# Performance work log

Hardware: AMD Instinct MI355X
Metric: run time of the kernel (lower is better)

Reference implementation:

```python
import jax, jax.numpy as jnp
import numpy as np


def setup_inputs() -> dict:
    key = jax.random.key(0)
    ks = jax.random.split(key, 10)
    B, C, T, H, W = 8, 128, 8, 32, 32
    Cq = C // 8
    return {
        "x": jax.random.normal(ks[0], (B, C, T, H, W), dtype=jnp.float32),
        "Wq": jax.random.normal(ks[1], (Cq, C), dtype=jnp.float32) * (1.0 / np.sqrt(C)),
        "bq": jax.random.normal(ks[2], (Cq,), dtype=jnp.float32) * 0.02,
        "Wk": jax.random.normal(ks[3], (Cq, C), dtype=jnp.float32) * (1.0 / np.sqrt(C)),
        "bk": jax.random.normal(ks[4], (Cq,), dtype=jnp.float32) * 0.02,
        "Wv": jax.random.normal(ks[5], (C, C), dtype=jnp.float32) * (1.0 / np.sqrt(C)),
        "bv": jax.random.normal(ks[6], (C,), dtype=jnp.float32) * 0.02,
        "gamma_pam": jax.random.normal(ks[7], (1,), dtype=jnp.float32),
        "gamma_cam": jax.random.normal(ks[8], (1,), dtype=jnp.float32),
        "gamma_tim": jax.random.normal(ks[9], (1,), dtype=jnp.float32),
    }


def reference(x, Wq, bq, Wk, bk, Wv, bv, gamma_pam, gamma_cam, gamma_tim):
    B, C, T, H, W = x.shape
    HW = H * W

    # ---- PAM: position attention over HW, feature dim = (C//8)*T ----
    # 1x1x1 Conv3d == per-position channel matmul
    q = jnp.einsum('bcthw,oc->bothw', x, Wq) + bq[None, :, None, None, None]
    k = jnp.einsum('bcthw,oc->bothw', x, Wk) + bk[None, :, None, None, None]
    v = jnp.einsum('bcthw,oc->bothw', x, Wv) + bv[None, :, None, None, None]
    qf = q.reshape(B, -1, HW)   # [B, (C//8)*T, HW]
    kf = k.reshape(B, -1, HW)
    vf = v.reshape(B, -1, HW)   # [B, C*T, HW]
    energy = jnp.einsum('bcn,bcm->bnm', qf, kf)          # [B, HW, HW]
    attn = jax.nn.softmax(energy, axis=-1)
    # out = bmm(v, attn^T)
    pam = jnp.einsum('bcm,bnm->bcn', vf, attn).reshape(B, C, T, H, W)
    pam = gamma_pam * pam + x

    # ---- CAM: channel attention (C x C) with negated-energy softmax ----
    xc = x.reshape(B, C, -1)                              # [B, C, T*HW]
    e = jnp.einsum('bcn,bdn->bcd', xc, xc)                # [B, C, C]
    e = jnp.max(e, axis=-1, keepdims=True) - e
    a = jax.nn.softmax(e, axis=-1)
    cam = jnp.einsum('bcd,bdn->bcn', a, xc).reshape(B, C, T, H, W)
    cam = gamma_cam * cam + x

    # ---- TIM: temporal attention (T x T) with negated-energy softmax ----
    xt = jnp.transpose(x, (0, 2, 1, 3, 4)).reshape(B, T, -1)  # [B, T, C*HW]
    e = jnp.einsum('btn,bsn->bts', xt, xt)                # [B, T, T]
    e = jnp.max(e, axis=-1, keepdims=True) - e
    a = jax.nn.softmax(e, axis=-1)
    tim = jnp.einsum('bts,bsn->btn', a, xt).reshape(B, T, C, H, W)
    tim = jnp.transpose(tim, (0, 2, 1, 3, 4))
    tim = gamma_tim * tim + x

    return pam + cam + tim
```

## Files before the change

### kernel.cpp

```cpp
#include <hip/hip_runtime.h>
#include <cstdint>

typedef unsigned short u16;
typedef __attribute__((ext_vector_type(8))) short bf16x8;
typedef __attribute__((ext_vector_type(4))) float f32x4;

constexpr int B_  = 8;
constexpr int C_  = 128;
constexpr int T_  = 8;
constexpr int HW_ = 1024;
constexpr int P_  = T_ * HW_;
constexpr int F_  = 128;
constexpr int CT_ = C_ * T_;

static __device__ __forceinline__ u16 f2bf(float f) {
    union { float f; unsigned u; } v; v.f = f;
    unsigned r = v.u + 0x7fffu + ((v.u >> 16) & 1u);
    return (u16)(r >> 16);
}
static __device__ __forceinline__ float bf2f(u16 h) {
    union { unsigned u; float f; } v; v.u = ((unsigned)h) << 16;
    return v.f;
}

#define GLOAD16(src, dst)                                                     \
    __builtin_amdgcn_global_load_lds(                                         \
        (const __attribute__((address_space(1))) void*)(src),                 \
        (__attribute__((address_space(3))) void*)(dst), 16, 0, 0)

__global__ __launch_bounds__(256)
void k_wcast(const float* __restrict__ Wq, const float* __restrict__ bq,
             const float* __restrict__ Wk, const float* __restrict__ bk,
             const float* __restrict__ Wv, const float* __restrict__ bv,
             u16* __restrict__ Wall, float* __restrict__ ball)
{
    int tid = blockIdx.x * 256 + threadIdx.x;
    if (tid < 20480) {
        int oc = tid >> 7, c = tid & 127;
        float w;
        if (oc < 16)      w = Wq[oc * 128 + c];
        else if (oc < 32) w = Wk[(oc - 16) * 128 + c];
        else              w = Wv[(oc - 32) * 128 + c];
        Wall[tid] = f2bf(w);
    }
    if (tid < 160) {
        float bb;
        if (tid < 16)      bb = bq[tid];
        else if (tid < 32) bb = bk[tid - 16];
        else               bb = bv[tid - 32];
        ball[tid] = bb;
    }
}

__global__ __launch_bounds__(256)
void k_prep(const float* __restrict__ x, u16* __restrict__ xT)
{
    __shared__ char sy[32768];
    const int b  = blockIdx.y;
    const int p0 = blockIdx.x * 128;
    const int tid = threadIdx.x;

    #pragma unroll
    for (int r = 0; r < 16; r++) {
        int lin = r * 256 + tid;
        int c = lin >> 5, j4 = (lin & 31) << 2;
        float4 xv = *(const float4*)&x[((size_t)(b * C_ + c)) * P_ + p0 + j4];
        float a4[4] = {xv.x, xv.y, xv.z, xv.w};
        #pragma unroll
        for (int u = 0; u < 4; u++) {
            int pi = j4 + u;
            int byte = pi * 256 + ((c * 2) ^ (((pi >> 2) & 15) << 4));
            *(u16*)(sy + byte) = f2bf(a4[u]);
        }
    }
    __syncthreads();
    #pragma unroll
    for (int r = 0; r < 8; r++) {
        int lin = r * 256 + tid;
        int pi = lin >> 4, ci8 = (lin & 15) << 3;
        bf16x8 v = *(const bf16x8*)(sy + pi * 256 +
                                    ((ci8 * 2) ^ (((pi >> 2) & 15) << 4)));
        *(bf16x8*)&xT[((size_t)(b * P_ + p0 + pi)) * C_ + ci8] = v;
    }
}

__global__ __launch_bounds__(256)
void k_qkv(const u16* __restrict__ xT, const u16* __restrict__ Wall,
           const float* __restrict__ ball,
           u16* __restrict__ qt, u16* __restrict__ kt, u16* __restrict__ v16)
{
    __shared__ char Ws[40960];
    const int b  = blockIdx.y;
    const int p0 = blockIdx.x * 128;
    const int tid = threadIdx.x, lane = tid & 63, w = tid >> 6;

    #pragma unroll
    for (int i = 0; i < 10; i++) {
        int ch  = w * 10 + i;
        int row = ch * 4 + (lane >> 4);
        int col = ((lane & 15) ^ (row & 7)) * 8;
        GLOAD16(Wall + row * 128 + col, Ws + ch * 1024);
    }

    const u16* Bb = xT + ((size_t)(b * P_ + p0 + w * 32)) * F_;
    bf16x8 bg[4][2];
    #pragma unroll
    for (int ks = 0; ks < 4; ks++)
        #pragma unroll
        for (int ni = 0; ni < 2; ni++)
            bg[ks][ni] = *(const bf16x8*)(Bb +
                (size_t)(ni * 16 + (lane & 15)) * F_ + ks * 32 + (lane >> 4) * 8);
    __syncthreads();

    f32x4 acc[10][2];
    #pragma unroll
    for (int mi = 0; mi < 10; mi++) {
        acc[mi][0] = (f32x4){0.f, 0.f, 0.f, 0.f};
        acc[mi][1] = (f32x4){0.f, 0.f, 0.f, 0.f};
    }

    #pragma unroll
    for (int mi = 0; mi < 10; mi++) {
        #pragma unroll
        for (int ks = 0; ks < 4; ks++) {
            int row  = mi * 16 + (lane & 15);
            int slot = (ks * 4 + (lane >> 4)) ^ (row & 7);
            bf16x8 af = *(const bf16x8*)(Ws + row * 256 + slot * 16);
            acc[mi][0] = __builtin_amdgcn_mfma_f32_16x16x32_bf16(
                af, bg[ks][0], acc[mi][0], 0, 0, 0);
            acc[mi][1] = __builtin_amdgcn_mfma_f32_16x16x32_bf16(
                af, bg[ks][1], acc[mi][1], 0, 0, 0);
        }
    }

    const int t      = p0 >> 10;
    const int hwbase = (p0 & 1023) + w * 32;
    #pragma unroll
    for (int mi = 0; mi < 10; mi++)
        #pragma unroll
        for (int ni = 0; ni < 2; ni++)
            #pragma unroll
            for (int r = 0; r < 4; r++) {
                int oc = mi * 16 + (lane >> 4) * 4 + r;
                int hw = hwbase + ni * 16 + (lane & 15);
                u16 bv16 = f2bf(acc[mi][ni][r] + ball[oc]);
                if (mi == 0)
                    qt[((size_t)b * HW_ + hw) * F_ + oc * 8 + t] = bv16;
                else if (mi == 1)
                    kt[((size_t)b * HW_ + hw) * F_ + (oc - 16) * 8 + t] = bv16;
                else
                    v16[((size_t)(b * C_ + oc - 32)) * P_ + t * HW_ + hw] = bv16;
            }
}

__global__ __launch_bounds__(256)
void k_energy(const u16* __restrict__ qt, const u16* __restrict__ kt,
              float* __restrict__ E)
{
    __shared__ char As[32768];
    __shared__ char Bs[32768];
    const int b  = blockIdx.z;
    const int n0 = blockIdx.y * 128, m0 = blockIdx.x * 128;
    const int tid = threadIdx.x, lane = tid & 63, w = tid >> 6;
    const u16* qb = qt + (size_t)b * HW_ * F_;
    const u16* kb = kt + (size_t)b * HW_ * F_;

    #pragma unroll
    for (int i = 0; i < 8; i++) {
        int c    = w * 8 + i;
        int row  = c * 4 + (lane >> 4);
        int col  = ((lane & 15) ^ (row & 7)) * 8;
        GLOAD16(qb + (size_t)(n0 + row) * F_ + col, As + c * 1024);
        GLOAD16(kb + (size_t)(m0 + row) * F_ + col, Bs + c * 1024);
    }
    __syncthreads();

    const int wr = w >> 1, wc = w & 1;
    f32x4 acc[4][4];
    #pragma unroll
    for (int mi = 0; mi < 4; mi++)
        #pragma unroll
        for (int ni = 0; ni < 4; ni++) acc[mi][ni] = (f32x4){0.f, 0.f, 0.f, 0.f};

    #pragma unroll
    for (int ks = 0; ks < 4; ks++) {
        bf16x8 af[4], bg[4];
        #pragma unroll
        for (int mi = 0; mi < 4; mi++) {
            int row  = wr * 64 + mi * 16 + (lane & 15);
            int slot = (ks * 4 + (lane >> 4)) ^ (row & 7);
            af[mi] = *(const bf16x8*)(As + row * 256 + slot * 16);
            int rb  = wc * 64 + mi * 16 + (lane & 15);
            int sb  = (ks * 4 + (lane >> 4)) ^ (rb & 7);
            bg[mi] = *(const bf16x8*)(Bs + rb * 256 + sb * 16);
        }
        #pragma unroll
        for (int mi = 0; mi < 4; mi++)
            #pragma unroll
            for (int ni = 0; ni < 4; ni++)
                acc[mi][ni] = __builtin_amdgcn_mfma_f32_16x16x32_bf16(
                    af[mi], bg[ni], acc[mi][ni], 0, 0, 0);
    }

    float* Eb = E + (size_t)b * HW_ * HW_;
    #pragma unroll
    for (int mi = 0; mi < 4; mi++)
        #pragma unroll
        for (int ni = 0; ni < 4; ni++)
            #pragma unroll
            for (int r = 0; r < 4; r++)
                Eb[(size_t)(n0 + wr * 64 + mi * 16 + (lane >> 4) * 4 + r) * HW_
                   + m0 + wc * 64 + ni * 16 + (lane & 15)] = acc[mi][ni][r];
}

__global__ __launch_bounds__(256)
void k_softmax(const float* __restrict__ E, u16* __restrict__ A16)
{
    const float* e = E + (size_t)blockIdx.x * HW_;
    const int tid = threadIdx.x;
    float4 v = ((const float4*)e)[tid];
    float m = fmaxf(fmaxf(v.x, v.y), fmaxf(v.z, v.w));
    #pragma unroll
    for (int off = 32; off; off >>= 1) m = fmaxf(m, __shfl_xor(m, off));
    __shared__ float s1[4], s2[4];
    if ((tid & 63) == 0) s1[tid >> 6] = m;
    __syncthreads();
    m = fmaxf(fmaxf(s1[0], s1[1]), fmaxf(s1[2], s1[3]));
    v.x = __expf(v.x - m); v.y = __expf(v.y - m);
    v.z = __expf(v.z - m); v.w = __expf(v.w - m);
    float s = v.x + v.y + v.z + v.w;
    #pragma unroll
    for (int off = 32; off; off >>= 1) s += __shfl_xor(s, off);
    if ((tid & 63) == 0) s2[tid >> 6] = s;
    __syncthreads();
    s = s2[0] + s2[1] + s2[2] + s2[3];
    float inv = 1.0f / s;
    ushort4 pk;
    pk.x = f2bf(v.x * inv); pk.y = f2bf(v.y * inv);
    pk.z = f2bf(v.z * inv); pk.w = f2bf(v.w * inv);
    ((ushort4*)(A16 + (size_t)blockIdx.x * HW_))[tid] = pk;
}

__global__ __launch_bounds__(256)
void k_pv(const u16* __restrict__ v16, const u16* __restrict__ A16,
          const float* __restrict__ gamma_pam, float* __restrict__ out)
{
    __shared__ char As[16384];
    __shared__ char Bs[16384];
    const int b   = blockIdx.z;
    const int ct0 = blockIdx.y * 128, n0 = blockIdx.x * 128;
    const int tid = threadIdx.x, lane = tid & 63, w = tid >> 6;
    const u16* vb = v16 + (size_t)b * CT_ * HW_;
    const u16* ab = A16 + (size_t)b * HW_ * HW_;

    const int wr = w >> 1, wc = w & 1;
    f32x4 acc[4][4];
    #pragma unroll
    for (int mi = 0; mi < 4; mi++)
        #pragma unroll
        for (int ni = 0; ni < 4; ni++) acc[mi][ni] = (f32x4){0.f, 0.f, 0.f, 0.f};

    for (int mc = 0; mc < 1024; mc += 64) {
        #pragma unroll
        for (int i = 0; i < 4; i++) {
            int c   = w * 4 + i;
            int row = c * 8 + (lane >> 3);
            int col = ((lane & 7) ^ (row & 7)) * 8;
            GLOAD16(vb + (size_t)(ct0 + row) * HW_ + mc + col, As + c * 1024);
            GLOAD16(ab + (size_t)(n0  + row) * HW_ + mc + col, Bs + c * 1024);
        }
        __syncthreads();
        #pragma unroll
        for (int ks = 0; ks < 2; ks++) {
            bf16x8 af[4], bg[4];
            #pragma unroll
            for (int mi = 0; mi < 4; mi++) {
                int row  = wr * 64 + mi * 16 + (lane & 15);
                int slot = (ks * 4 + (lane >> 4)) ^ (row & 7);
                af[mi] = *(const bf16x8*)(As + row * 128 + slot * 16);
                int rb  = wc * 64 + mi * 16 + (lane & 15);
                int sb  = (ks * 4 + (lane >> 4)) ^ (rb & 7);
                bg[mi] = *(const bf16x8*)(Bs + rb * 128 + sb * 16);
            }
            #pragma unroll
            for (int mi = 0; mi < 4; mi++)
                #pragma unroll
                for (int ni = 0; ni < 4; ni++)
                    acc[mi][ni] = __builtin_amdgcn_mfma_f32_16x16x32_bf16(
                        af[mi], bg[ni], acc[mi][ni], 0, 0, 0);
        }
        __syncthreads();
    }

    const float gp = gamma_pam[0];
    float* ob = out + (size_t)b * CT_ * HW_;
    #pragma unroll
    for (int mi = 0; mi < 4; mi++)
        #pragma unroll
        for (int ni = 0; ni < 4; ni++)
            #pragma unroll
            for (int r = 0; r < 4; r++)
                ob[(size_t)(ct0 + wr * 64 + mi * 16 + (lane >> 4) * 4 + r) * HW_
                   + n0 + wc * 64 + ni * 16 + (lane & 15)] = gp * acc[mi][ni][r];
}

__global__ __launch_bounds__(256)
void k_split(const float* __restrict__ x, u16* __restrict__ xhi,
             u16* __restrict__ xlo)
{
    for (int i = blockIdx.x * 256 + threadIdx.x; i < 2097152; i += 2048 * 256) {
        float4 v = ((const float4*)x)[i];
        ushort4 h, l;
        h.x = f2bf(v.x); h.y = f2bf(v.y); h.z = f2bf(v.z); h.w = f2bf(v.w);
        l.x = f2bf(v.x - bf2f(h.x)); l.y = f2bf(v.y - bf2f(h.y));
        l.z = f2bf(v.z - bf2f(h.z)); l.w = f2bf(v.w - bf2f(h.w));
        ((ushort4*)xhi)[i] = h;
        ((ushort4*)xlo)[i] = l;
    }
}

__global__ __launch_bounds__(256)
void k_cam_gram(const u16* __restrict__ xhi, const u16* __restrict__ xlo,
                float* __restrict__ part)
{
    __shared__ char Sh[32768];
    __shared__ char Sl[32768];
    const int b = blockIdx.y, ch = blockIdx.x;
    const int tid = threadIdx.x, lane = tid & 63, w = tid >> 6;
    const u16* hb = xhi + (size_t)b * C_ * P_;
    const u16* lb = xlo + (size_t)b * C_ * P_;

    f32x4 acc[8][2];
    #pragma unroll
    for (int mi = 0; mi < 8; mi++) {
        acc[mi][0] = (f32x4){0.f, 0.f, 0.f, 0.f};
        acc[mi][1] = (f32x4){0.f, 0.f, 0.f, 0.f};
    }

    for (int kc = 0; kc < 2; kc++) {
        int n0 = ch * 256 + kc * 128;
        #pragma unroll
        for (int i = 0; i < 8; i++) {
            int c4  = w * 8 + i;
            int row = c4 * 4 + (lane >> 4);
            int col = ((lane & 15) ^ (row & 7)) * 8;
            GLOAD16(hb + (size_t)row * P_ + n0 + col, Sh + c4 * 1024);
            GLOAD16(lb + (size_t)row * P_ + n0 + col, Sl + c4 * 1024);
        }
        __syncthreads();
        #pragma unroll
        for (int ks = 0; ks < 4; ks++) {
            bf16x8 bh[2], bl[2];
            #pragma unroll
            for (int ni = 0; ni < 2; ni++) {
                int rb = w * 32 + ni * 16 + (lane & 15);
                int sb = (ks * 4 + (lane >> 4)) ^ (rb & 7);
                bh[ni] = *(const bf16x8*)(Sh + rb * 256 + sb * 16);
                bl[ni] = *(const bf16x8*)(Sl + rb * 256 + sb * 16);
            }
            #pragma unroll
            for (int mi = 0; mi < 8; mi++) {
                int ra = mi * 16 + (lane & 15);
                int sa = (ks * 4 + (lane >> 4)) ^ (ra & 7);
                bf16x8 ah = *(const bf16x8*)(Sh + ra * 256 + sa * 16);
                bf16x8 al = *(const bf16x8*)(Sl + ra * 256 + sa * 16);
                #pragma unroll
                for (int ni = 0; ni < 2; ni++) {
                    acc[mi][ni] = __builtin_amdgcn_mfma_f32_16x16x32_bf16(
                        ah, bh[ni], acc[mi][ni], 0, 0, 0);
                    acc[mi][ni] = __builtin_amdgcn_mfma_f32_16x16x32_bf16(
                        ah, bl[ni], acc[mi][ni], 0, 0, 0);
                    acc[mi][ni] = __builtin_amdgcn_mfma_f32_16x16x32_bf16(
                        al, bh[ni], acc[mi][ni], 0, 0, 0);
                }
            }
        }
        __syncthreads();
    }

    float* pb = part + ((size_t)(b * 32 + ch)) * 16384;
    #pragma unroll
    for (int mi = 0; mi < 8; mi++)
        #pragma unroll
        for (int ni = 0; ni < 2; ni++)
            #pragma unroll
            for (int r = 0; r < 4; r++) {
                int c = mi * 16 + (lane >> 4) * 4 + r;
                int d = w * 32 + ni * 16 + (lane & 15);
                pb[c * 128 + d] = acc[mi][ni][r];
            }
}

__global__ __launch_bounds__(128)
void k_cam_reduce(const float* __restrict__ part,
                  const float* __restrict__ gamma_cam, u16* __restrict__ acam16)
{
    const int b = blockIdx.y, c = blockIdx.x;
    const int d = threadIdx.x;
    float s = 0.f;
    for (int ch = 0; ch < 32; ch++)
        s += part[(((size_t)(b * 32 + ch)) * C_ + c) * C_ + d];
    float mn = s;
    #pragma unroll
    for (int off = 32; off; off >>= 1) mn = fminf(mn, __shfl_xor(mn, off));
    __shared__ float m1[2], m2[2];
    if ((d & 63) == 0) m1[d >> 6] = mn;
    __syncthreads();
    mn = fminf(m1[0], m1[1]);
    float p = __expf(mn - s);
    float sum = p;
    #pragma unroll
    for (int off = 32; off; off >>= 1) sum += __shfl_xor(sum, off);
    if ((d & 63) == 0) m2[d >> 6] = sum;
    __syncthreads();
    sum = m2[0] + m2[1];
    acam16[((size_t)(b * C_ + c)) * C_ + d] = f2bf(gamma_cam[0] * p / sum);
}

__global__ __launch_bounds__(256)
void k_tim_gram(const float* __restrict__ x, float* __restrict__ e_t)
{
    const int b = blockIdx.y, c = blockIdx.x;
    const int tid = threadIdx.x;
    const float* xb = x + ((size_t)(b * C_ + c)) * P_;
    float acc[8][8] = {};
    for (int r = 0; r < 4; r++) {
        int hw = r * 256 + tid;
        float xv[8];
        #pragma unroll
        for (int t = 0; t < 8; t++) xv[t] = xb[t * HW_ + hw];
        #pragma unroll
        for (int t = 0; t < 8; t++)
            #pragma unroll
            for (int s2 = 0; s2 < 8; s2++)
                acc[t][s2] += xv[t] * xv[s2];
    }
    __shared__ float sm[4][64];
    const int lane = tid & 63, wid = tid >> 6;
    #pragma unroll
    for (int u = 0; u < 64; u++) {
        float vv = acc[u >> 3][u & 7];
        #pragma unroll
        for (int off = 32; off; off >>= 1) vv += __shfl_xor(vv, off);
        if (lane == 0) sm[wid][u] = vv;
    }
    __syncthreads();
    if (tid < 64) {
        float vv = sm[0][tid] + sm[1][tid] + sm[2][tid] + sm[3][tid];
        atomicAdd(&e_t[b * 64 + tid], vv);
    }
}

__global__ __launch_bounds__(512)
void k_tim_softmax(const float* __restrict__ e_t, float* __restrict__ a_t)
{
    const int tid = threadIdx.x;
    float v = e_t[tid];
    float mn = v;
    #pragma unroll
    for (int off = 4; off; off >>= 1) mn = fminf(mn, __shfl_xor(mn, off, 8));
    float p = __expf(mn - v);
    float s = p;
    #pragma unroll
    for (int off = 4; off; off >>= 1) s += __shfl_xor(s, off, 8);
    a_t[tid] = p / s;
}

__global__ __launch_bounds__(256)
void k_xprime(const float* __restrict__ x, const float* __restrict__ atim,
              const float* __restrict__ gamma_tim, u16* __restrict__ Xp)
{
    const int b = blockIdx.y, c = blockIdx.x;
    const size_t base = ((size_t)(b * C_ + c)) * P_;
    const int tid = threadIdx.x;
    const float gt = gamma_tim[0];

    float4 xv[8];
    #pragma unroll
    for (int t = 0; t < 8; t++)
        xv[t] = *(const float4*)&x[base + t * HW_ + tid * 4];

    #pragma unroll
    for (int t = 0; t < 8; t++) {
        float4 o = make_float4(3.f * xv[t].x, 3.f * xv[t].y,
                               3.f * xv[t].z, 3.f * xv[t].w);
        #pragma unroll
        for (int s = 0; s < 8; s++) {
            float w = gt * atim[b * 64 + t * 8 + s];
            o.x += w * xv[s].x; o.y += w * xv[s].y;
            o.z += w * xv[s].z; o.w += w * xv[s].w;
        }
        ushort4 pk;
        pk.x = f2bf(o.x); pk.y = f2bf(o.y); pk.z = f2bf(o.z); pk.w = f2bf(o.w);
        *(ushort4*)&Xp[base + t * HW_ + tid * 4] = pk;
    }
}

__global__ __launch_bounds__(256)
void k_cam_av(const u16* __restrict__ acam16, const u16* __restrict__ xT,
              const u16* __restrict__ Xp, float* __restrict__ out)
{
    const int b  = blockIdx.y;
    const int p0 = blockIdx.x * 128;
    const int tid = threadIdx.x, lane = tid & 63, w = tid >> 6;

    const u16* Ab = acam16 + (size_t)b * C_ * C_;
    const u16* Bb = xT + ((size_t)(b * P_ + p0 + w * 32)) * C_;

    f32x4 acc[8][2];
    #pragma unroll
    for (int mi = 0; mi < 8; mi++) {
        acc[mi][0] = (f32x4){0.f, 0.f, 0.f, 0.f};
        acc[mi][1] = (f32x4){0.f, 0.f, 0.f, 0.f};
    }

    bf16x8 bg[4][2];
    #pragma unroll
    for (int ks = 0; ks < 4; ks++)
        #pragma unroll
        for (int ni = 0; ni < 2; ni++)
            bg[ks][ni] = *(const bf16x8*)(Bb +
                (size_t)(ni * 16 + (lane & 15)) * C_ + ks * 32 + (lane >> 4) * 8);

    #pragma unroll
    for (int mi = 0; mi < 8; mi++) {
        #pragma unroll
        for (int ks = 0; ks < 4; ks++) {
            bf16x8 af = *(const bf16x8*)(Ab +
                (size_t)(mi * 16 + (lane & 15)) * C_ + ks * 32 + (lane >> 4) * 8);
            acc[mi][0] = __builtin_amdgcn_mfma_f32_16x16x32_bf16(
                af, bg[ks][0], acc[mi][0], 0, 0, 0);
            acc[mi][1] = __builtin_amdgcn_mfma_f32_16x16x32_bf16(
                af, bg[ks][1], acc[mi][1], 0, 0, 0);
        }
    }

    float* ob = out + (size_t)b * C_ * P_;
    const u16* xp = Xp + (size_t)b * C_ * P_;
    #pragma unroll
    for (int mi = 0; mi < 8; mi++)
        #pragma unroll
        for (int ni = 0; ni < 2; ni++)
            #pragma unroll
            for (int r = 0; r < 4; r++) {
                int c = mi * 16 + (lane >> 4) * 4 + r;
                int p = p0 + w * 32 + ni * 16 + (lane & 15);
                size_t i = (size_t)c * P_ + p;
                ob[i] += acc[mi][ni][r] + bf2f(xp[i]);
            }
}

extern "C" void kernel_launch(void* const* d_in, const int* in_sizes, int n_in,
                              void* d_out, int out_size, void* d_ws, size_t ws_size,
                              hipStream_t stream)
{
    (void)in_sizes; (void)n_in; (void)out_size; (void)ws_size;
    const float* x  = (const float*)d_in[0];
    const float* Wq = (const float*)d_in[1];
    const float* bq = (const float*)d_in[2];
    const float* Wk = (const float*)d_in[3];
    const float* bk = (const float*)d_in[4];
    const float* Wv = (const float*)d_in[5];
    const float* bv = (const float*)d_in[6];
    const float* gp = (const float*)d_in[7];
    const float* gc = (const float*)d_in[8];
    const float* gt = (const float*)d_in[9];
    float* out = (float*)d_out;
    char*  ws  = (char*)d_ws;

    const size_t MiB = 1u << 20;
    u16*   xT     = (u16*)(ws + 0);
    u16*   qtb    = (u16*)(ws + 16 * MiB);
    u16*   ktb    = (u16*)(ws + 18 * MiB);
    u16*   v16    = (u16*)(ws + 20 * MiB);
    u16*   Xp16   = (u16*)(ws + 20 * MiB);
    float* Ebuf   = (float*)(ws + 36 * MiB);
    u16*   xhi    = (u16*)(ws + 36 * MiB);
    u16*   xlo    = (u16*)(ws + 52 * MiB);
    u16*   A16    = (u16*)(ws + 68 * MiB);
    float* part   = (float*)(ws + 68 * MiB);
    u16*   acam16 = (u16*)(ws + 84 * MiB);
    u16*   Wall   = (u16*)(ws + 84 * MiB + 65536);
    float* ball   = (float*)(ws + 84 * MiB + 131072);
    float* etim   = (float*)(ws + 84 * MiB + 139264);
    float* atim   = (float*)(ws + 84 * MiB + 143360);

    hipMemsetAsync(etim, 0, 512 * sizeof(float), stream);

    k_wcast      <<<dim3(80),      256, 0, stream>>>(Wq, bq, Wk, bk, Wv, bv,
                                                     Wall, ball);
    k_prep       <<<dim3(64, 8),   256, 0, stream>>>(x, xT);
    k_qkv        <<<dim3(64, 8),   256, 0, stream>>>(xT, Wall, ball,
                                                     qtb, ktb, v16);
    k_energy     <<<dim3(8, 8, 8), 256, 0, stream>>>(qtb, ktb, Ebuf);
    k_softmax    <<<dim3(8192),    256, 0, stream>>>(Ebuf, A16);
    k_split      <<<dim3(2048),    256, 0, stream>>>(x, xhi, xlo);
    k_tim_gram   <<<dim3(128, 8),  256, 0, stream>>>(x, etim);
    k_tim_softmax<<<dim3(1),       512, 0, stream>>>(etim, atim);
    k_pv         <<<dim3(8, 8, 8), 256, 0, stream>>>(v16, A16, gp, out);
    k_xprime     <<<dim3(128, 8),  256, 0, stream>>>(x, atim, gt, Xp16);
    k_cam_gram   <<<dim3(32, 8),   256, 0, stream>>>(xhi, xlo, part);
    k_cam_reduce <<<dim3(128, 8),  128, 0, stream>>>(part, gc, acam16);
    k_cam_av     <<<dim3(64, 8),   256, 0, stream>>>(acam16, xT, Xp16, out);
}
```

Baseline: 263.4 us.

## Fuse prep kernels, double-buffer PV GEMM, and store PAM as bf16

Folds the weight cast and the hi/lo bf16 split of x into the prep kernel, and moves the temporal softmax into k_xprime. This removes three launches and one full extra pass over x. The PV GEMM now double-buffers its LDS tiles so global loads for the next step overlap the MFMA work on the current one. PAM output is written as bf16 to a scratch buffer and added in the final CAM kernel, which replaces the fp32 read-modify-write of out with a single store. The cost is reduced PAM precision, twice the LDS in k_pv, and a strided gather of PAM values in the epilogue.

New measurement: 266.1 us. No clear change (+1.0%).

```diff
diff --git a/kernel.cpp b/kernel.cpp
--- a/kernel.cpp
+++ b/kernel.cpp
@@ -29,48 +29,58 @@
         (__attribute__((address_space(3))) void*)(dst), 16, 0, 0)
 
 __global__ __launch_bounds__(256)
-void k_wcast(const float* __restrict__ Wq, const float* __restrict__ bq,
-             const float* __restrict__ Wk, const float* __restrict__ bk,
-             const float* __restrict__ Wv, const float* __restrict__ bv,
-             u16* __restrict__ Wall, float* __restrict__ ball)
-{
-    int tid = blockIdx.x * 256 + threadIdx.x;
-    if (tid < 20480) {
-        int oc = tid >> 7, c = tid & 127;
-        float w;
-        if (oc < 16)      w = Wq[oc * 128 + c];
-        else if (oc < 32) w = Wk[(oc - 16) * 128 + c];
-        else              w = Wv[(oc - 32) * 128 + c];
-        Wall[tid] = f2bf(w);
-    }
-    if (tid < 160) {
-        float bb;
-        if (tid < 16)      bb = bq[tid];
-        else if (tid < 32) bb = bk[tid - 16];
-        else               bb = bv[tid - 32];
-        ball[tid] = bb;
-    }
-}
-
-__global__ __launch_bounds__(256)
-void k_prep(const float* __restrict__ x, u16* __restrict__ xT)
-{
+void k_prep(const float* __restrict__ x, u16* __restrict__ xT,
+            u16* __restrict__ xhi, u16* __restrict__ xlo,
+            const float* __restrict__ Wq, const float* __restrict__ bq,
+            const float* __restrict__ Wk, const float* __restrict__ bk,
+            const float* __restrict__ Wv, const float* __restrict__ bv,
+            u16* __restrict__ Wall, float* __restrict__ ball)
+{
+    const int tid = threadIdx.x;
+    if (blockIdx.x == 64) {
+        if (blockIdx.y != 0) return;
+        for (int i = tid; i < 20480; i += 256) {
+            int oc = i >> 7, c = i & 127;
+            float w;
+            if (oc < 16)      w = Wq[oc * 128 + c];
+            else if (oc < 32) w = Wk[(oc - 16) * 128 + c];
+            else              w = Wv[(oc - 32) * 128 + c];
+            Wall[i] = f2bf(w);
+        }
+        if (tid < 160) {
+            float bb;
+            if (tid < 16)      bb = bq[tid];
+            else if (tid < 32) bb = bk[tid - 16];
+            else               bb = bv[tid - 32];
+            ball[tid] = bb;
+        }
+        return;
+    }
+
     __shared__ char sy[32768];
     const int b  = blockIdx.y;
     const int p0 = blockIdx.x * 128;
-    const int tid = threadIdx.x;
 
     #pragma unroll
     for (int r = 0; r < 16; r++) {
         int lin = r * 256 + tid;
         int c = lin >> 5, j4 = (lin & 31) << 2;
-        float4 xv = *(const float4*)&x[((size_t)(b * C_ + c)) * P_ + p0 + j4];
+        size_t gi = ((size_t)(b * C_ + c)) * P_ + p0 + j4;
+        float4 xv = *(const float4*)&x[gi];
         float a4[4] = {xv.x, xv.y, xv.z, xv.w};
+        ushort4 h, l;
+        h.x = f2bf(a4[0]); h.y = f2bf(a4[1]);
+        h.z = f2bf(a4[2]); h.w = f2bf(a4[3]);
+        l.x = f2bf(a4[0] - bf2f(h.x)); l.y = f2bf(a4[1] - bf2f(h.y));
+        l.z = f2bf(a4[2] - bf2f(h.z)); l.w = f2bf(a4[3] - bf2f(h.w));
+        *(ushort4*)&xhi[gi] = h;
+        *(ushort4*)&xlo[gi] = l;
         #pragma unroll
         for (int u = 0; u < 4; u++) {
             int pi = j4 + u;
             int byte = pi * 256 + ((c * 2) ^ (((pi >> 2) & 15) << 4));
-            *(u16*)(sy + byte) = f2bf(a4[u]);
+            *(u16*)(sy + byte) = (u == 0) ? h.x : (u == 1) ? h.y
+                               : (u == 2) ? h.z : h.w;
         }
     }
     __syncthreads();
@@ -243,16 +253,19 @@
 
 __global__ __launch_bounds__(256)
 void k_pv(const u16* __restrict__ v16, const u16* __restrict__ A16,
-          const float* __restrict__ gamma_pam, float* __restrict__ out)
-{
-    __shared__ char As[16384];
-    __shared__ char Bs[16384];
+          const float* __restrict__ gamma_pam, u16* __restrict__ pam16)
+{
+    __shared__ char As[2][16384];
+    __shared__ char Bs[2][16384];
     const int b   = blockIdx.z;
     const int ct0 = blockIdx.y * 128, n0 = blockIdx.x * 128;
     const int tid = threadIdx.x, lane = tid & 63, w = tid >> 6;
     const u16* vb = v16 + (size_t)b * CT_ * HW_;
     const u16* ab = A16 + (size_t)b * HW_ * HW_;
 
+    const int s_row = (lane >> 3);
+    const int s_col = ((lane & 7) ^ ((lane >> 3) & 7)) * 8;
+
     const int wr = w >> 1, wc = w & 1;
     f32x4 acc[4][4];
     #pragma unroll
@@ -260,16 +273,31 @@
         #pragma unroll
         for (int ni = 0; ni < 4; ni++) acc[mi][ni] = (f32x4){0.f, 0.f, 0.f, 0.f};
 
-    for (int mc = 0; mc < 1024; mc += 64) {
-        #pragma unroll
-        for (int i = 0; i < 4; i++) {
-            int c   = w * 4 + i;
-            int row = c * 8 + (lane >> 3);
-            int col = ((lane & 7) ^ (row & 7)) * 8;
-            GLOAD16(vb + (size_t)(ct0 + row) * HW_ + mc + col, As + c * 1024);
-            GLOAD16(ab + (size_t)(n0  + row) * HW_ + mc + col, Bs + c * 1024);
-        }
-        __syncthreads();
+    #pragma unroll
+    for (int i = 0; i < 4; i++) {
+        int c = w * 4 + i;
+        int row = c * 8 + s_row;
+        GLOAD16(vb + (size_t)(ct0 + row) * HW_ + s_col, As[0] + c * 1024);
+        GLOAD16(ab + (size_t)(n0  + row) * HW_ + s_col, Bs[0] + c * 1024);
+    }
+    __syncthreads();
+
+    int cur = 0;
+    for (int it = 0; it < 16; ++it) {
+        if (it < 15) {
+            int mc = (it + 1) * 64;
+            #pragma unroll
+            for (int i = 0; i < 4; i++) {
+                int c = w * 4 + i;
+                int row = c * 8 + s_row;
+                GLOAD16(vb + (size_t)(ct0 + row) * HW_ + mc + s_col,
+                        As[cur ^ 1] + c * 1024);
+                GLOAD16(ab + (size_t)(n0  + row) * HW_ + mc + s_col,
+                        Bs[cur ^ 1] + c * 1024);
+            }
+        }
+        const char* Ac = As[cur];
+        const char* Bc = Bs[cur];
         #pragma unroll
         for (int ks = 0; ks < 2; ks++) {
             bf16x8 af[4], bg[4];
@@ -277,10 +305,10 @@
             for (int mi = 0; mi < 4; mi++) {
                 int row  = wr * 64 + mi * 16 + (lane & 15);
                 int slot = (ks * 4 + (lane >> 4)) ^ (row & 7);
-                af[mi] = *(const bf16x8*)(As + row * 128 + slot * 16);
+                af[mi] = *(const bf16x8*)(Ac + row * 128 + slot * 16);
                 int rb  = wc * 64 + mi * 16 + (lane & 15);
                 int sb  = (ks * 4 + (lane >> 4)) ^ (rb & 7);
-                bg[mi] = *(const bf16x8*)(Bs + rb * 128 + sb * 16);
+                bg[mi] = *(const bf16x8*)(Bc + rb * 128 + sb * 16);
             }
             #pragma unroll
             for (int mi = 0; mi < 4; mi++)
@@ -290,10 +318,11 @@
                         af[mi], bg[ni], acc[mi][ni], 0, 0, 0);
         }
         __syncthreads();
+        cur ^= 1;
     }
 
     const float gp = gamma_pam[0];
-    float* ob = out + (size_t)b * CT_ * HW_;
+    u16* ob = pam16 + (size_t)b * CT_ * HW_;
     #pragma unroll
     for (int mi = 0; mi < 4; mi++)
         #pragma unroll
@@ -301,22 +330,8 @@
             #pragma unroll
             for (int r = 0; r < 4; r++)
                 ob[(size_t)(ct0 + wr * 64 + mi * 16 + (lane >> 4) * 4 + r) * HW_
-                   + n0 + wc * 64 + ni * 16 + (lane & 15)] = gp * acc[mi][ni][r];
-}
-
-__global__ __launch_bounds__(256)
-void k_split(const float* __restrict__ x, u16* __restrict__ xhi,
-             u16* __restrict__ xlo)
-{
-    for (int i = blockIdx.x * 256 + threadIdx.x; i < 2097152; i += 2048 * 256) {
-        float4 v = ((const float4*)x)[i];
-        ushort4 h, l;
-        h.x = f2bf(v.x); h.y = f2bf(v.y); h.z = f2bf(v.z); h.w = f2bf(v.w);
-        l.x = f2bf(v.x - bf2f(h.x)); l.y = f2bf(v.y - bf2f(h.y));
-        l.z = f2bf(v.z - bf2f(h.z)); l.w = f2bf(v.w - bf2f(h.w));
-        ((ushort4*)xhi)[i] = h;
-        ((ushort4*)xlo)[i] = l;
-    }
+                   + n0 + wc * 64 + ni * 16 + (lane & 15)] =
+                    f2bf(gp * acc[mi][ni][r]);
 }
 
 __global__ __launch_bounds__(256)
@@ -451,23 +466,8 @@
     }
 }
 
-__global__ __launch_bounds__(512)
-void k_tim_softmax(const float* __restrict__ e_t, float* __restrict__ a_t)
-{
-    const int tid = threadIdx.x;
-    float v = e_t[tid];
-    float mn = v;
-    #pragma unroll
-    for (int off = 4; off; off >>= 1) mn = fminf(mn, __shfl_xor(mn, off, 8));
-    float p = __expf(mn - v);
-    float s = p;
-    #pragma unroll
-    for (int off = 4; off; off >>= 1) s += __shfl_xor(s, off, 8);
-    a_t[tid] = p / s;
-}
-
-__global__ __launch_bounds__(256)
-void k_xprime(const float* __restrict__ x, const float* __restrict__ atim,
+__global__ __launch_bounds__(256)
+void k_xprime(const float* __restrict__ x, const float* __restrict__ e_t,
               const float* __restrict__ gamma_tim, u16* __restrict__ Xp)
 {
     const int b = blockIdx.y, c = blockIdx.x;
@@ -482,13 +482,24 @@
 
     #pragma unroll
     for (int t = 0; t < 8; t++) {
+        float e[8];
+        #pragma unroll
+        for (int s = 0; s < 8; s++) e[s] = e_t[b * 64 + t * 8 + s];
+        float mn = e[0];
+        #pragma unroll
+        for (int s = 1; s < 8; s++) mn = fminf(mn, e[s]);
+        float p[8], sum = 0.f;
+        #pragma unroll
+        for (int s = 0; s < 8; s++) { p[s] = __expf(mn - e[s]); sum += p[s]; }
+        float inv = gt / sum;
+
         float4 o = make_float4(3.f * xv[t].x, 3.f * xv[t].y,
                                3.f * xv[t].z, 3.f * xv[t].w);
         #pragma unroll
         for (int s = 0; s < 8; s++) {
-            float w = gt * atim[b * 64 + t * 8 + s];
-            o.x += w * xv[s].x; o.y += w * xv[s].y;
-            o.z += w * xv[s].z; o.w += w * xv[s].w;
+            float wgt = p[s] * inv;
+            o.x += wgt * xv[s].x; o.y += wgt * xv[s].y;
+            o.z += wgt * xv[s].z; o.w += wgt * xv[s].w;
         }
         ushort4 pk;
         pk.x = f2bf(o.x); pk.y = f2bf(o.y); pk.z = f2bf(o.z); pk.w = f2bf(o.w);
@@ -498,7 +509,8 @@
 
 __global__ __launch_bounds__(256)
 void k_cam_av(const u16* __restrict__ acam16, const u16* __restrict__ xT,
-              const u16* __restrict__ Xp, float* __restrict__ out)
+              const u16* __restrict__ Xp, const u16* __restrict__ pam16,
+              float* __restrict__ out)
 {
     const int b  = blockIdx.y;
     const int p0 = blockIdx.x * 128;
@@ -535,8 +547,10 @@
         }
     }
 
+    const int tt = p0 >> 10;
     float* ob = out + (size_t)b * C_ * P_;
     const u16* xp = Xp + (size_t)b * C_ * P_;
+    const u16* pb = pam16 + (size_t)b * CT_ * HW_;
     #pragma unroll
     for (int mi = 0; mi < 8; mi++)
         #pragma unroll
@@ -545,8 +559,10 @@
             for (int r = 0; r < 4; r++) {
                 int c = mi * 16 + (lane >> 4) * 4 + r;
                 int p = p0 + w * 32 + ni * 16 + (lane & 15);
+                int hw = p & 1023;
                 size_t i = (size_t)c * P_ + p;
-                ob[i] += acc[mi][ni][r] + bf2f(xp[i]);
+                float pam = bf2f(pb[((size_t)(c * 8 + tt)) * HW_ + hw]);
+                ob[i] = pam + acc[mi][ni][r] + bf2f(xp[i]);
             }
 }
 
@@ -570,36 +586,35 @@
 
     const size_t MiB = 1u << 20;
     u16*   xT     = (u16*)(ws + 0);
-    u16*   qtb    = (u16*)(ws + 16 * MiB);
-    u16*   ktb    = (u16*)(ws + 18 * MiB);
-    u16*   v16    = (u16*)(ws + 20 * MiB);
-    u16*   Xp16   = (u16*)(ws + 20 * MiB);
-    float* Ebuf   = (float*)(ws + 36 * MiB);
-    u16*   xhi    = (u16*)(ws + 36 * MiB);
-    u16*   xlo    = (u16*)(ws + 52 * MiB);
-    u16*   A16    = (u16*)(ws + 68 * MiB);
-    float* part   = (float*)(ws + 68 * MiB);
-    u16*   acam16 = (u16*)(ws + 84 * MiB);
-    u16*   Wall   = (u16*)(ws + 84 * MiB + 65536);
-    float* ball   = (float*)(ws + 84 * MiB + 131072);
-    float* etim   = (float*)(ws + 84 * MiB + 139264);
-    float* atim   = (float*)(ws + 84 * MiB + 143360);
+    u16*   v16    = (u16*)(ws + 16 * MiB);
+    u16*   xhi    = (u16*)(ws + 32 * MiB);
+    u16*   xlo    = (u16*)(ws + 48 * MiB);
+    float* Ebuf   = (float*)(ws + 64 * MiB);
+    float* part   = (float*)(ws + 64 * MiB);
+    u16*   pam16  = (u16*)(ws + 80 * MiB);
+    u16*   A16    = (u16*)(ws + 96 * MiB);
+    u16*   Xp16   = (u16*)(ws + 96 * MiB);
+    u16*   qtb    = (u16*)(ws + 112 * MiB);
+    u16*   ktb    = (u16*)(ws + 114 * MiB);
+    u16*   acam16 = (u16*)(ws + 116 * MiB);
+    u16*   Wall   = (u16*)(ws + 116 * MiB + 65536);
+    float* ball   = (float*)(ws + 116 * MiB + 131072);
+    float* etim   = (float*)(ws + 116 * MiB + 139264);
 
     hipMemsetAsync(etim, 0, 512 * sizeof(float), stream);
 
-    k_wcast      <<<dim3(80),      256, 0, stream>>>(Wq, bq, Wk, bk, Wv, bv,
-                                                     Wall, ball);
-    k_prep       <<<dim3(64, 8),   256, 0, stream>>>(x, xT);
-    k_qkv        <<<dim3(64, 8),   256, 0, stream>>>(xT, Wall, ball,
-                                                     qtb, ktb, v16);
-    k_energy     <<<dim3(8, 8, 8), 256, 0, stream>>>(qtb, ktb, Ebuf);
-    k_softmax    <<<dim3(8192),    256, 0, stream>>>(Ebuf, A16);
-    k_split      <<<dim3(2048),    256, 0, stream>>>(x, xhi, xlo);
-    k_tim_gram   <<<dim3(128, 8),  256, 0, stream>>>(x, etim);
-    k_tim_softmax<<<dim3(1),       512, 0, stream>>>(etim, atim);
-    k_pv         <<<dim3(8, 8, 8), 256, 0, stream>>>(v16, A16, gp, out);
-    k_xprime     <<<dim3(128, 8),  256, 0, stream>>>(x, atim, gt, Xp16);
-    k_cam_gram   <<<dim3(32, 8),   256, 0, stream>>>(xhi, xlo, part);
-    k_cam_reduce <<<dim3(128, 8),  128, 0, stream>>>(part, gc, acam16);
-    k_cam_av     <<<dim3(64, 8),   256, 0, stream>>>(acam16, xT, Xp16, out);
-}
+    k_prep      <<<dim3(65, 8),   256, 0, stream>>>(x, xT, xhi, xlo,
+                                                    Wq, bq, Wk, bk, Wv, bv,
+                                                    Wall, ball);
+    k_qkv       <<<dim3(64, 8),   256, 0, stream>>>(xT, Wall, ball,
+                                                    qtb, ktb, v16);
+    k_energy    <<<dim3(8, 8, 8), 256, 0, stream>>>(qtb, ktb, Ebuf);
+    k_softmax   <<<dim3(8192),    256, 0, stream>>>(Ebuf, A16);
+    k_tim_gram  <<<dim3(128, 8),  256, 0, stream>>>(x, etim);
+    k_pv        <<<dim3(8, 8, 8), 256, 0, stream>>>(v16, A16, gp, pam16);
+    k_xprime    <<<dim3(128, 8),  256, 0, stream>>>(x, etim, gt, Xp16);
+    k_cam_gram  <<<dim3(32, 8),   256, 0, stream>>>(xhi, xlo, part);
+    k_cam_reduce<<<dim3(128, 8),  128, 0, stream>>>(part, gc, acam16);
+    k_cam_av    <<<dim3(64, 8),   256, 0, stream>>>(acam16, xT, Xp16,
+                                                    pam16, out);
+}
```
